# Kernel tuning notes

Measured on AMD Instinct MI355X. Metric: run time of the kernel, lower is better.

## Reference

```python
import jax, jax.numpy as jnp
import numpy as np

D_K = 24
ALPHA = 0.1
N_HEADS = 6
D_MODEL = 144
LN_EPS = 1e-5


def setup_inputs() -> dict:
    key = jax.random.key(0)
    ks = jax.random.split(key, 8)
    B, S = 8, 2048
    Q = jax.random.normal(ks[0], (B, S, D_MODEL), dtype=jnp.float32)
    K = jax.random.normal(ks[1], (B, N_HEADS, S, D_K), dtype=jnp.float32)
    V = jax.random.normal(ks[2], (B, N_HEADS, S, D_K), dtype=jnp.float32)
    attn_mask = jax.random.randint(ks[3], (B, S, S), 0, 2).astype(bool)
    Wq_w = jax.random.normal(ks[4], (D_MODEL, D_MODEL), dtype=jnp.float32) * 0.05
    Wq_b = jnp.zeros((D_MODEL,), dtype=jnp.float32)
    lin_w = jax.random.normal(ks[5], (D_MODEL, D_MODEL), dtype=jnp.float32) * 0.05
    lin_b = jnp.zeros((D_MODEL,), dtype=jnp.float32)
    ln_g = jnp.ones((D_MODEL,), dtype=jnp.float32)
    ln_b = jnp.zeros((D_MODEL,), dtype=jnp.float32)
    return {"Q": Q, "K": K, "V": V, "attn_mask": attn_mask,
            "Wq_w": Wq_w, "Wq_b": Wq_b, "lin_w": lin_w, "lin_b": lin_b,
            "ln_g": ln_g, "ln_b": ln_b}


def reference(Q, K, V, attn_mask, Wq_w, Wq_b, lin_w, lin_b, ln_g, ln_b):
    B, S, _ = Q.shape
    residual = Q
    # W_Q projection then head split: [B,S,D] -> [B,H,S,d_k]
    q = (Q @ Wq_w.T + Wq_b).reshape(B, S, N_HEADS, D_K).transpose(0, 2, 1, 3)
    # scores [B,H,S,Sk]; custom tanh activation instead of softmax
    scores = jnp.einsum('bhqd,bhkd->bhqk', q, K) / np.sqrt(D_K).astype(np.float32)
    attn = jnp.tanh(ALPHA * scores)
    # NOTE: original calls attn.masked_fill(...) non-inplace and drops the
    # result, so attn_mask has no effect. Faithfully ignored here.
    context = jnp.einsum('bhqk,bhkd->bhqd', attn, V)
    context = context.transpose(0, 2, 1, 3).reshape(B, S, N_HEADS * D_K)
    output = context @ lin_w.T + lin_b
    x = output + residual
    mu = jnp.mean(x, axis=-1, keepdims=True)
    var = jnp.var(x, axis=-1, keepdims=True)
    return (x - mu) / jnp.sqrt(var + LN_EPS) * ln_g + ln_b
```

## Files before the change

### kernel.cpp

```cpp
#include <hip/hip_runtime.h>
#include <hip/hip_bf16.h>

#define B_  8
#define S_  2048
#define H_  6
#define DK_ 24
#define DM_ 144

#define TK0  2.0412414523193153e-02f
#define TK1 -2.8350575726379381e-06f
#define TK2  4.7250959543965635e-10f
#define TK3 -7.9686705934386491e-14f

typedef __bf16 bf16x8 __attribute__((ext_vector_type(8)));
typedef __bf16 bf16x2 __attribute__((ext_vector_type(2)));
typedef float  f32x4  __attribute__((ext_vector_type(4)));

__device__ __forceinline__ unsigned short f2bf(float f) {
    return __builtin_bit_cast(unsigned short, (__bf16)f);
}
__device__ __forceinline__ uint pack2(float a, float b) {
    bf16x2 v; v[0] = (__bf16)a; v[1] = (__bf16)b;
    return __builtin_bit_cast(uint, v);
}
__device__ __forceinline__ float tanh_s(float c) {
    float t = c * c;
    float u = fmaf(t, TK3, TK2);
    u = fmaf(t, u, TK1);
    u = fmaf(t, u, TK0);
    return c * u;
}

__global__ __launch_bounds__(256)
void prep_w_kernel(const float* __restrict__ Wq, const float* __restrict__ Wqb,
                   const float* __restrict__ Wl, const float* __restrict__ lb,
                   ushort* __restrict__ Whq, ushort* __restrict__ Wlp) {
    int i = blockIdx.x * 256 + threadIdx.x;
    if (i < 30720) {
        int h = i / 5120, rem = i % 5120;
        int d = rem / 160, c = rem % 160;
        float v = 0.f;
        if (d < DK_) {
            if (c < DM_)       v = Wq[(h * DK_ + d) * DM_ + c];
            else if (c == DM_) v = Wqb[h * DK_ + d];
        }
        Whq[i] = f2bf(v);
    } else if (i < 53760) {
        int j = i - 30720;
        int r = j / 160, c = j % 160;
        float v = (c < DM_) ? Wl[r * DM_ + c] : (c == DM_ ? lb[r] : 0.f);
        Wlp[j] = f2bf(v);
    }
}

__global__ __launch_bounds__(256)
void prep_kv_kernel(const float* __restrict__ K, const float* __restrict__ V,
                    ushort* __restrict__ Ktt, ushort* __restrict__ Vtt) {
    __shared__ float sv[64 * 25];
    const int t = threadIdx.x;
    const int kt = blockIdx.x, h = blockIdx.y, b = blockIdx.z;
    const int bh = b * H_ + h;
    const size_t tile = (size_t)(bh * 32 + kt);
    const float4* Ks = (const float4*)(K + ((size_t)bh * S_ + kt * 64) * DK_);
    ushort* Ko = Ktt + tile * 2048;
    for (int idx = t; idx < 384; idx += 256) {
        int r = idx / 6, c4 = (idx % 6) * 4;
        float4 v = Ks[idx];
        ushort4 u; u.x = f2bf(v.x); u.y = f2bf(v.y); u.z = f2bf(v.z); u.w = f2bf(v.w);
        *(ushort4*)&Ko[r * 32 + c4] = u;
    }
    if (t < 64) { uint4 z = {0u,0u,0u,0u}; *(uint4*)&Ko[t * 32 + 24] = z; }
    const float4* Vs = (const float4*)(V + ((size_t)bh * S_ + kt * 64) * DK_);
    for (int idx = t; idx < 384; idx += 256) {
        int r = idx / 6, c4 = (idx % 6) * 4;
        *(float4*)&sv[r * 25 + c4] = Vs[idx];
    }
    __syncthreads();
    int d = t >> 3, s8 = (t & 7) * 8;
    uint4 o = {0u,0u,0u,0u};
    if (d < DK_) {
        o.x = pack2(sv[(s8 + 0) * 25 + d], sv[(s8 + 1) * 25 + d]);
        o.y = pack2(sv[(s8 + 2) * 25 + d], sv[(s8 + 3) * 25 + d]);
        o.z = pack2(sv[(s8 + 4) * 25 + d], sv[(s8 + 5) * 25 + d]);
        o.w = pack2(sv[(s8 + 6) * 25 + d], sv[(s8 + 7) * 25 + d]);
    }
    ((uint4*)Vtt)[tile * 256 + t] = o;
}

__global__ __launch_bounds__(256)
void attn_kernel(const float* __restrict__ Q, const ushort* __restrict__ Whq,
                 const ushort* __restrict__ Ktt, const ushort* __restrict__ Vtt,
                 float* __restrict__ out) {
    __shared__ __attribute__((aligned(16))) char smem[42496];
    ushort* s_q  = (ushort*)smem;
    ushort* s_k  = (ushort*)(smem + 10240);
    ushort* s_vt = (ushort*)(smem + 20480);
    ushort* s_p  = (ushort*)(smem + 29696);
    ushort* s_a  = (ushort*)(smem + 10240);
    ushort* s_w  = (ushort*)(smem + 31744);
    float*  s_ctx= (float*)(smem + 10240);

    const int t = threadIdx.x;
    const int w = t >> 6, n16 = t & 15, g = (t >> 4) & 3;
    const int qp = blockIdx.x, h = blockIdx.y, b = blockIdx.z;
    const int bh = b * H_ + h;
    const int row0 = qp * 128;

    const uint4* Kb = (const uint4*)(Ktt + (size_t)bh * 65536);
    const uint4* Vb = (const uint4*)(Vtt + (size_t)bh * 65536);
    uint4 kv = Kb[t], vv = Vb[t];

    const uint4* Ws = (const uint4*)(Whq + h * 5120);
    for (int idx = t; idx < 640; idx += 256) {
        int r = idx / 20, c8 = (idx % 20) * 8;
        *(uint4*)&s_w[r * 168 + c8] = Ws[idx];
    }
    const f32x4 zf = {0.f, 0.f, 0.f, 0.f};
#pragma unroll
    for (int pass = 0; pass < 2; ++pass) {
        const float4* Qs = (const float4*)(Q + ((size_t)b * S_ + row0 + pass * 64) * DM_);
        for (int idx = t; idx < 2304; idx += 256) {
            int r = idx / 36, c4 = (idx % 36) * 4;
            float4 v = Qs[idx];
            uint2 u; u.x = pack2(v.x, v.y); u.y = pack2(v.z, v.w);
            *(uint2*)&s_a[r * 168 + c4] = u;
        }
        if (t < 64) {
            uint4 pad = {0x00003F80u, 0u, 0u, 0u};
            uint4 z4  = {0u, 0u, 0u, 0u};
            *(uint4*)&s_a[t * 168 + 144] = pad;
            *(uint4*)&s_a[t * 168 + 152] = z4;
        }
        __syncthreads();
        f32x4 qa0 = zf, qa1 = zf;
#pragma unroll
        for (int ks = 0; ks < 5; ++ks) {
            bf16x8 av = *(const bf16x8*)&s_a[(w * 16 + n16) * 168 + ks * 32 + g * 8];
            bf16x8 b0 = *(const bf16x8*)&s_w[n16 * 168 + ks * 32 + g * 8];
            bf16x8 b1 = *(const bf16x8*)&s_w[(16 + n16) * 168 + ks * 32 + g * 8];
            qa0 = __builtin_amdgcn_mfma_f32_16x16x32_bf16(av, b0, qa0, 0, 0, 0);
            qa1 = __builtin_amdgcn_mfma_f32_16x16x32_bf16(av, b1, qa1, 0, 0, 0);
        }
#pragma unroll
        for (int reg = 0; reg < 4; ++reg) {
            int r = (pass * 64 + w * 16 + g * 4 + reg) * 40;
            s_q[r + n16]      = f2bf(qa0[reg]);
            s_q[r + 16 + n16] = f2bf(qa1[reg]);
        }
        __syncthreads();
    }

    const bf16x8 qf0 = *(const bf16x8*)&s_q[(w * 16 + n16) * 40 + g * 8];
    const bf16x8 qf1 = *(const bf16x8*)&s_q[(64 + w * 16 + n16) * 40 + g * 8];

    const int koff = (t >> 2) * 40 + (t & 3) * 8;
    const int voff = (t >> 3) * 72 + (t & 7) * 8;
    const int prow = (w * 16 + n16) * 72;

    f32x4 acc00 = zf, acc01 = zf, acc10 = zf, acc11 = zf;
    int p = 0;
    for (int kt = 0; kt < 32; ++kt) {
        *(uint4*)&s_k[p * 2560 + koff] = kv;
        *(uint4*)&s_vt[p * 2304 + voff] = vv;
        __syncthreads();
        {
            int nt = (kt + 1) & 31;
            kv = Kb[nt * 256 + t];
            vv = Vb[nt * 256 + t];
        }
        bf16x8 a0 = *(const bf16x8*)&s_k[p * 2560 + n16 * 40 + g * 8];
        bf16x8 a1 = *(const bf16x8*)&s_k[p * 2560 + (16 + n16) * 40 + g * 8];
        bf16x8 a2 = *(const bf16x8*)&s_k[p * 2560 + (32 + n16) * 40 + g * 8];
        bf16x8 a3 = *(const bf16x8*)&s_k[p * 2560 + (48 + n16) * 40 + g * 8];
        bf16x8 vb00 = *(const bf16x8*)&s_vt[p * 2304 + n16 * 72 + g * 8];
        bf16x8 vb01 = *(const bf16x8*)&s_vt[p * 2304 + (16 + n16) * 72 + g * 8];
        bf16x8 vb10 = *(const bf16x8*)&s_vt[p * 2304 + n16 * 72 + 32 + g * 8];
        bf16x8 vb11 = *(const bf16x8*)&s_vt[p * 2304 + (16 + n16) * 72 + 32 + g * 8];
        {
            f32x4 c0 = __builtin_amdgcn_mfma_f32_16x16x32_bf16(a0, qf0, zf, 0, 0, 0);
            f32x4 c1 = __builtin_amdgcn_mfma_f32_16x16x32_bf16(a1, qf0, zf, 0, 0, 0);
            f32x4 c2 = __builtin_amdgcn_mfma_f32_16x16x32_bf16(a2, qf0, zf, 0, 0, 0);
            f32x4 c3 = __builtin_amdgcn_mfma_f32_16x16x32_bf16(a3, qf0, zf, 0, 0, 0);
            uint2 u;
            u.x = pack2(tanh_s(c0[0]), tanh_s(c0[1]));
            u.y = pack2(tanh_s(c0[2]), tanh_s(c0[3]));
            *(uint2*)&s_p[prow + 0  + g * 4] = u;
            u.x = pack2(tanh_s(c1[0]), tanh_s(c1[1]));
            u.y = pack2(tanh_s(c1[2]), tanh_s(c1[3]));
            *(uint2*)&s_p[prow + 16 + g * 4] = u;
            u.x = pack2(tanh_s(c2[0]), tanh_s(c2[1]));
            u.y = pack2(tanh_s(c2[2]), tanh_s(c2[3]));
            *(uint2*)&s_p[prow + 32 + g * 4] = u;
            u.x = pack2(tanh_s(c3[0]), tanh_s(c3[1]));
            u.y = pack2(tanh_s(c3[2]), tanh_s(c3[3]));
            *(uint2*)&s_p[prow + 48 + g * 4] = u;
            bf16x8 ap0 = *(const bf16x8*)&s_p[prow + g * 8];
            acc00 = __builtin_amdgcn_mfma_f32_16x16x32_bf16(ap0, vb00, acc00, 0, 0, 0);
            acc01 = __builtin_amdgcn_mfma_f32_16x16x32_bf16(ap0, vb01, acc01, 0, 0, 0);
            bf16x8 ap1 = *(const bf16x8*)&s_p[prow + 32 + g * 8];
            acc00 = __builtin_amdgcn_mfma_f32_16x16x32_bf16(ap1, vb10, acc00, 0, 0, 0);
            acc01 = __builtin_amdgcn_mfma_f32_16x16x32_bf16(ap1, vb11, acc01, 0, 0, 0);
        }
        {
            f32x4 c0 = __builtin_amdgcn_mfma_f32_16x16x32_bf16(a0, qf1, zf, 0, 0, 0);
            f32x4 c1 = __builtin_amdgcn_mfma_f32_16x16x32_bf16(a1, qf1, zf, 0, 0, 0);
            f32x4 c2 = __builtin_amdgcn_mfma_f32_16x16x32_bf16(a2, qf1, zf, 0, 0, 0);
            f32x4 c3 = __builtin_amdgcn_mfma_f32_16x16x32_bf16(a3, qf1, zf, 0, 0, 0);
            uint2 u;
            u.x = pack2(tanh_s(c0[0]), tanh_s(c0[1]));
            u.y = pack2(tanh_s(c0[2]), tanh_s(c0[3]));
            *(uint2*)&s_p[prow + 0  + g * 4] = u;
            u.x = pack2(tanh_s(c1[0]), tanh_s(c1[1]));
            u.y = pack2(tanh_s(c1[2]), tanh_s(c1[3]));
            *(uint2*)&s_p[prow + 16 + g * 4] = u;
            u.x = pack2(tanh_s(c2[0]), tanh_s(c2[1]));
            u.y = pack2(tanh_s(c2[2]), tanh_s(c2[3]));
            *(uint2*)&s_p[prow + 32 + g * 4] = u;
            u.x = pack2(tanh_s(c3[0]), tanh_s(c3[1]));
            u.y = pack2(tanh_s(c3[2]), tanh_s(c3[3]));
            *(uint2*)&s_p[prow + 48 + g * 4] = u;
            bf16x8 ap0 = *(const bf16x8*)&s_p[prow + g * 8];
            acc10 = __builtin_amdgcn_mfma_f32_16x16x32_bf16(ap0, vb00, acc10, 0, 0, 0);
            acc11 = __builtin_amdgcn_mfma_f32_16x16x32_bf16(ap0, vb01, acc11, 0, 0, 0);
            bf16x8 ap1 = *(const bf16x8*)&s_p[prow + 32 + g * 8];
            acc10 = __builtin_amdgcn_mfma_f32_16x16x32_bf16(ap1, vb10, acc10, 0, 0, 0);
            acc11 = __builtin_amdgcn_mfma_f32_16x16x32_bf16(ap1, vb11, acc11, 0, 0, 0);
        }
        p ^= 1;
    }

    __syncthreads();
#pragma unroll
    for (int reg = 0; reg < 4; ++reg) {
        int row = w * 16 + g * 4 + reg;
        s_ctx[row * 28 + n16] = acc00[reg];
        if (n16 < 8) s_ctx[row * 28 + 16 + n16] = acc01[reg];
        s_ctx[(64 + row) * 28 + n16] = acc10[reg];
        if (n16 < 8) s_ctx[(64 + row) * 28 + 16 + n16] = acc11[reg];
    }
    __syncthreads();
    for (int idx = t; idx < 768; idx += 256) {
        int r = idx / 6, c = idx % 6;
        float4 v4 = *(const float4*)&s_ctx[r * 28 + c * 4];
        *(float4*)&out[((size_t)b * S_ + row0 + r) * DM_ + h * DK_ + c * 4] = v4;
    }
}

__global__ __launch_bounds__(512)
void outln_kernel(const float* __restrict__ Qres, const ushort* __restrict__ Wlp,
                  const float* __restrict__ lg, const float* __restrict__ lbeta,
                  float* __restrict__ io) {
    __shared__ __attribute__((aligned(16))) ushort s_a[64 * 168];
    __shared__ __attribute__((aligned(16))) ushort s_w[144 * 168];
    __shared__ float s_red[2][2][64];
    const int t = threadIdx.x;
    const int w = t >> 6, n16 = t & 15, g = (t >> 4) & 3;
    const int wq = w & 3, half = w >> 2;
    const int nt_base = half * 5, nt_cnt = half ? 4 : 5;
    const int row0 = blockIdx.x * 64;

    for (int idx = t; idx < 2304; idx += 512) {
        int r = idx / 36, c4 = (idx % 36) * 4;
        float4 v = *(const float4*)&io[(size_t)(row0 + r) * DM_ + c4];
        uint2 u; u.x = pack2(v.x, v.y); u.y = pack2(v.z, v.w);
        *(uint2*)&s_a[r * 168 + c4] = u;
    }
    if (t < 64) {
        uint4 pad = {0x00003F80u, 0u, 0u, 0u};
        uint4 z4  = {0u, 0u, 0u, 0u};
        *(uint4*)&s_a[t * 168 + 144] = pad;
        *(uint4*)&s_a[t * 168 + 152] = z4;
    }
    for (int idx = t; idx < 2880; idx += 512) {
        int r = idx / 20, c8 = (idx % 20) * 8;
        *(uint4*)&s_w[r * 168 + c8] = *(const uint4*)&Wlp[r * 160 + c8];
    }
    __syncthreads();

    f32x4 acc[5];
#pragma unroll
    for (int j = 0; j < 5; ++j) acc[j] = (f32x4){0.f, 0.f, 0.f, 0.f};
#pragma unroll
    for (int ks = 0; ks < 5; ++ks) {
        bf16x8 av = *(const bf16x8*)&s_a[(wq * 16 + n16) * 168 + ks * 32 + g * 8];
        for (int j = 0; j < nt_cnt; ++j) {
            bf16x8 bv = *(const bf16x8*)&s_w[((nt_base + j) * 16 + n16) * 168 + ks * 32 + g * 8];
            acc[j] = __builtin_amdgcn_mfma_f32_16x16x32_bf16(av, bv, acc[j], 0, 0, 0);
        }
    }
    float vals[5][4], s1[4] = {0, 0, 0, 0}, s2[4] = {0, 0, 0, 0};
    for (int j = 0; j < nt_cnt; ++j) {
        int d = (nt_base + j) * 16 + n16;
#pragma unroll
        for (int reg = 0; reg < 4; ++reg) {
            int row = row0 + wq * 16 + g * 4 + reg;
            float v = acc[j][reg] + Qres[(size_t)row * DM_ + d];
            vals[j][reg] = v;
            s1[reg] += v; s2[reg] = fmaf(v, v, s2[reg]);
        }
    }
#pragma unroll
    for (int off = 1; off < 16; off <<= 1) {
#pragma unroll
        for (int reg = 0; reg < 4; ++reg) {
            s1[reg] += __shfl_xor(s1[reg], off);
            s2[reg] += __shfl_xor(s2[reg], off);
        }
    }
    if (n16 == 0) {
#pragma unroll
        for (int reg = 0; reg < 4; ++reg) {
            int rr = wq * 16 + g * 4 + reg;
            s_red[half][0][rr] = s1[reg];
            s_red[half][1][rr] = s2[reg];
        }
    }
    __syncthreads();
    float mu[4], rs[4];
#pragma unroll
    for (int reg = 0; reg < 4; ++reg) {
        int rr = wq * 16 + g * 4 + reg;
        float S1 = s_red[0][0][rr] + s_red[1][0][rr];
        float S2 = s_red[0][1][rr] + s_red[1][1][rr];
        float m = S1 * (1.f / 144.f);
        mu[reg] = m;
        rs[reg] = rsqrtf(S2 * (1.f / 144.f) - m * m + 1e-5f);
    }
    for (int j = 0; j < nt_cnt; ++j) {
        int d = (nt_base + j) * 16 + n16;
        float gv = lg[d], bv = lbeta[d];
#pragma unroll
        for (int reg = 0; reg < 4; ++reg) {
            int row = row0 + wq * 16 + g * 4 + reg;
            io[(size_t)row * DM_ + d] = (vals[j][reg] - mu[reg]) * rs[reg] * gv + bv;
        }
    }
}

extern "C" void kernel_launch(void* const* d_in, const int* in_sizes, int n_in,
                              void* d_out, int out_size, void* d_ws, size_t ws_size,
                              hipStream_t stream) {
    const float* Q     = (const float*)d_in[0];
    const float* K     = (const float*)d_in[1];
    const float* V     = (const float*)d_in[2];
    const float* Wq_w  = (const float*)d_in[4];
    const float* Wq_b  = (const float*)d_in[5];
    const float* lin_w = (const float*)d_in[6];
    const float* lin_b = (const float*)d_in[7];
    const float* ln_g  = (const float*)d_in[8];
    const float* ln_b  = (const float*)d_in[9];
    float* out = (float*)d_out;

    ushort* Ktt = (ushort*)d_ws;
    ushort* Vtt = (ushort*)((char*)d_ws + 6291456);
    ushort* Whq = (ushort*)((char*)d_ws + 12582912);
    ushort* Wlp = (ushort*)((char*)d_ws + 12644352);

    prep_w_kernel<<<210, 256, 0, stream>>>(Wq_w, Wq_b, lin_w, lin_b, Whq, Wlp);
    prep_kv_kernel<<<dim3(32, H_, B_), 256, 0, stream>>>(K, V, Ktt, Vtt);
    attn_kernel<<<dim3(S_ / 128, H_, B_), 256, 0, stream>>>(Q, Whq, Ktt, Vtt, out);
    outln_kernel<<<(B_ * S_) / 64, 512, 0, stream>>>(Q, Wlp, ln_g, ln_b, out);
}
```

Before: 270.0 us.

## Load K/V fragments directly to registers and software-pipeline attention per wave

The attention loop stops staging K and V tiles through shared memory with block-wide barriers. Each wave now loads its MFMA fragments straight from global memory into double-buffered registers. A per-wave double-buffered P scratch lets the P·V MFMAs of one tile overlap the QK MFMAs of the next. The Q projection also reads Q and the weights directly from global memory, the tanh polynomial drops its highest-order term, and launch bounds request three blocks per CU. These changes remove barriers and LDS traffic, at the cost of more registers, redundant global loads per wave, and a slightly less accurate tanh.

Result: slower. 281.5 us (+4.3%).

```diff
diff --git a/kernel.cpp b/kernel.cpp
--- a/kernel.cpp
+++ b/kernel.cpp
@@ -10,12 +10,13 @@
 #define TK0  2.0412414523193153e-02f
 #define TK1 -2.8350575726379381e-06f
 #define TK2  4.7250959543965635e-10f
-#define TK3 -7.9686705934386491e-14f
 
 typedef __bf16 bf16x8 __attribute__((ext_vector_type(8)));
 typedef __bf16 bf16x2 __attribute__((ext_vector_type(2)));
 typedef float  f32x4  __attribute__((ext_vector_type(4)));
 
+#define MFMA_ __builtin_amdgcn_mfma_f32_16x16x32_bf16
+
 __device__ __forceinline__ unsigned short f2bf(float f) {
     return __builtin_bit_cast(unsigned short, (__bf16)f);
 }
@@ -25,8 +26,7 @@
 }
 __device__ __forceinline__ float tanh_s(float c) {
     float t = c * c;
-    float u = fmaf(t, TK3, TK2);
-    u = fmaf(t, u, TK1);
+    float u = fmaf(t, TK2, TK1);
     u = fmaf(t, u, TK0);
     return c * u;
 }
@@ -87,18 +87,77 @@
     ((uint4*)Vtt)[tile * 256 + t] = o;
 }
 
-__global__ __launch_bounds__(256)
+template<int PQ, bool DO_PV, bool PRE>
+__device__ __forceinline__ void attn_step(
+    int kt, const uint4* __restrict__ Kb4, const uint4* __restrict__ Vb4,
+    int koff, int voff, ushort* s_pw, int prow, int g,
+    const bf16x8& qf0, const bf16x8& qf1,
+    bf16x8 (&kf)[2][4], bf16x8 (&vf)[2][4],
+    f32x4& acc00, f32x4& acc01, f32x4& acc10, f32x4& acc11)
+{
+    constexpr int OP = 1 - PQ;
+    const f32x4 zf = {0.f, 0.f, 0.f, 0.f};
+    if (PRE) {
+        const int tb = ((kt + 1) & 31) * 256;
+#pragma unroll
+        for (int mt = 0; mt < 4; ++mt)
+            kf[OP][mt] = __builtin_bit_cast(bf16x8, Kb4[tb + mt * 64 + koff]);
+    }
+    bf16x8 ap00, ap01, ap10, ap11;
+    if (DO_PV) {
+        const ushort* pr = s_pw + OP * 2304 + prow;
+        ap00 = *(const bf16x8*)&pr[g * 8];
+        ap01 = *(const bf16x8*)&pr[32 + g * 8];
+        ap10 = *(const bf16x8*)&pr[1152 + g * 8];
+        ap11 = *(const bf16x8*)&pr[1152 + 32 + g * 8];
+    }
+    f32x4 c0[4], c1[4];
+#pragma unroll
+    for (int mt = 0; mt < 4; ++mt) c0[mt] = MFMA_(kf[PQ][mt], qf0, zf, 0, 0, 0);
+#pragma unroll
+    for (int mt = 0; mt < 4; ++mt) c1[mt] = MFMA_(kf[PQ][mt], qf1, zf, 0, 0, 0);
+    if (DO_PV) {
+        acc00 = MFMA_(ap00, vf[OP][0], acc00, 0, 0, 0);
+        acc00 = MFMA_(ap01, vf[OP][1], acc00, 0, 0, 0);
+        acc01 = MFMA_(ap00, vf[OP][2], acc01, 0, 0, 0);
+        acc01 = MFMA_(ap01, vf[OP][3], acc01, 0, 0, 0);
+        acc10 = MFMA_(ap10, vf[OP][0], acc10, 0, 0, 0);
+        acc10 = MFMA_(ap11, vf[OP][1], acc10, 0, 0, 0);
+        acc11 = MFMA_(ap10, vf[OP][2], acc11, 0, 0, 0);
+        acc11 = MFMA_(ap11, vf[OP][3], acc11, 0, 0, 0);
+    }
+    if (PRE) {
+        const int tb = ((kt + 1) & 31) * 256;
+#pragma unroll
+        for (int j = 0; j < 4; ++j)
+            vf[OP][j] = __builtin_bit_cast(bf16x8,
+                Vb4[tb + (j >> 1) * 128 + (j & 1) * 4 + voff]);
+    }
+    ushort* pw = s_pw + PQ * 2304 + prow;
+#pragma unroll
+    for (int mt = 0; mt < 4; ++mt) {
+        uint2 u;
+        u.x = pack2(tanh_s(c0[mt][0]), tanh_s(c0[mt][1]));
+        u.y = pack2(tanh_s(c0[mt][2]), tanh_s(c0[mt][3]));
+        *(uint2*)&pw[mt * 16 + g * 4] = u;
+    }
+#pragma unroll
+    for (int mt = 0; mt < 4; ++mt) {
+        uint2 u;
+        u.x = pack2(tanh_s(c1[mt][0]), tanh_s(c1[mt][1]));
+        u.y = pack2(tanh_s(c1[mt][2]), tanh_s(c1[mt][3]));
+        *(uint2*)&pw[1152 + mt * 16 + g * 4] = u;
+    }
+}
+
+__global__ __launch_bounds__(256, 3)
 void attn_kernel(const float* __restrict__ Q, const ushort* __restrict__ Whq,
                  const ushort* __restrict__ Ktt, const ushort* __restrict__ Vtt,
                  float* __restrict__ out) {
-    __shared__ __attribute__((aligned(16))) char smem[42496];
-    ushort* s_q  = (ushort*)smem;
-    ushort* s_k  = (ushort*)(smem + 10240);
-    ushort* s_vt = (ushort*)(smem + 20480);
-    ushort* s_p  = (ushort*)(smem + 29696);
-    ushort* s_a  = (ushort*)(smem + 10240);
-    ushort* s_w  = (ushort*)(smem + 31744);
-    float*  s_ctx= (float*)(smem + 10240);
+    __shared__ __attribute__((aligned(16))) char smem[47104];
+    ushort* s_q = (ushort*)smem;
+    ushort* s_p = (ushort*)(smem + 10240);
+    float*  s_ctx = (float*)(smem + 10240);
 
     const int t = threadIdx.x;
     const int w = t >> 6, n16 = t & 15, g = (t >> 4) & 3;
@@ -106,40 +165,44 @@
     const int bh = b * H_ + h;
     const int row0 = qp * 128;
 
-    const uint4* Kb = (const uint4*)(Ktt + (size_t)bh * 65536);
-    const uint4* Vb = (const uint4*)(Vtt + (size_t)bh * 65536);
-    uint4 kv = Kb[t], vv = Vb[t];
-
-    const uint4* Ws = (const uint4*)(Whq + h * 5120);
-    for (int idx = t; idx < 640; idx += 256) {
-        int r = idx / 20, c8 = (idx % 20) * 8;
-        *(uint4*)&s_w[r * 168 + c8] = Ws[idx];
-    }
+    const uint4* Kb4 = (const uint4*)Ktt + (size_t)bh * 8192;
+    const uint4* Vb4 = (const uint4*)Vtt + (size_t)bh * 8192;
+    const int koff = n16 * 4 + g;
+    const int voff = n16 * 8 + g;
+
+    bf16x8 kf[2][4], vf[2][4];
+#pragma unroll
+    for (int mt = 0; mt < 4; ++mt)
+        kf[0][mt] = __builtin_bit_cast(bf16x8, Kb4[mt * 64 + koff]);
+#pragma unroll
+    for (int j = 0; j < 4; ++j)
+        vf[0][j] = __builtin_bit_cast(bf16x8, Vb4[(j >> 1) * 128 + (j & 1) * 4 + voff]);
+
     const f32x4 zf = {0.f, 0.f, 0.f, 0.f};
+    const uint4* Wh4 = (const uint4*)Whq + h * 640;
 #pragma unroll
     for (int pass = 0; pass < 2; ++pass) {
-        const float4* Qs = (const float4*)(Q + ((size_t)b * S_ + row0 + pass * 64) * DM_);
-        for (int idx = t; idx < 2304; idx += 256) {
-            int r = idx / 36, c4 = (idx % 36) * 4;
-            float4 v = Qs[idx];
-            uint2 u; u.x = pack2(v.x, v.y); u.y = pack2(v.z, v.w);
-            *(uint2*)&s_a[r * 168 + c4] = u;
-        }
-        if (t < 64) {
-            uint4 pad = {0x00003F80u, 0u, 0u, 0u};
-            uint4 z4  = {0u, 0u, 0u, 0u};
-            *(uint4*)&s_a[t * 168 + 144] = pad;
-            *(uint4*)&s_a[t * 168 + 152] = z4;
-        }
-        __syncthreads();
+        const float* Qr = Q + (size_t)(b * S_ + row0 + pass * 64 + w * 16 + n16) * DM_;
         f32x4 qa0 = zf, qa1 = zf;
 #pragma unroll
         for (int ks = 0; ks < 5; ++ks) {
-            bf16x8 av = *(const bf16x8*)&s_a[(w * 16 + n16) * 168 + ks * 32 + g * 8];
-            bf16x8 b0 = *(const bf16x8*)&s_w[n16 * 168 + ks * 32 + g * 8];
-            bf16x8 b1 = *(const bf16x8*)&s_w[(16 + n16) * 168 + ks * 32 + g * 8];
-            qa0 = __builtin_amdgcn_mfma_f32_16x16x32_bf16(av, b0, qa0, 0, 0, 0);
-            qa1 = __builtin_amdgcn_mfma_f32_16x16x32_bf16(av, b1, qa1, 0, 0, 0);
+            bf16x8 av;
+            if (ks < 4 || g < 2) {
+                float4 f0 = *(const float4*)&Qr[ks * 32 + g * 8];
+                float4 f1 = *(const float4*)&Qr[ks * 32 + g * 8 + 4];
+                uint4 u;
+                u.x = pack2(f0.x, f0.y); u.y = pack2(f0.z, f0.w);
+                u.z = pack2(f1.x, f1.y); u.w = pack2(f1.z, f1.w);
+                av = __builtin_bit_cast(bf16x8, u);
+            } else {
+                uint4 u = {0u, 0u, 0u, 0u};
+                if (g == 2) u.x = 0x00003F80u;
+                av = __builtin_bit_cast(bf16x8, u);
+            }
+            bf16x8 bv0 = __builtin_bit_cast(bf16x8, Wh4[n16 * 20 + ks * 4 + g]);
+            bf16x8 bv1 = __builtin_bit_cast(bf16x8, Wh4[(16 + n16) * 20 + ks * 4 + g]);
+            qa0 = MFMA_(av, bv0, qa0, 0, 0, 0);
+            qa1 = MFMA_(av, bv1, qa1, 0, 0, 0);
         }
 #pragma unroll
         for (int reg = 0; reg < 4; ++reg) {
@@ -147,86 +210,38 @@
             s_q[r + n16]      = f2bf(qa0[reg]);
             s_q[r + 16 + n16] = f2bf(qa1[reg]);
         }
-        __syncthreads();
-    }
-
+    }
     const bf16x8 qf0 = *(const bf16x8*)&s_q[(w * 16 + n16) * 40 + g * 8];
     const bf16x8 qf1 = *(const bf16x8*)&s_q[(64 + w * 16 + n16) * 40 + g * 8];
 
-    const int koff = (t >> 2) * 40 + (t & 3) * 8;
-    const int voff = (t >> 3) * 72 + (t & 7) * 8;
-    const int prow = (w * 16 + n16) * 72;
-
+    ushort* s_pw = s_p + w * 4608;
+    const int prow = n16 * 72;
     f32x4 acc00 = zf, acc01 = zf, acc10 = zf, acc11 = zf;
-    int p = 0;
-    for (int kt = 0; kt < 32; ++kt) {
-        *(uint4*)&s_k[p * 2560 + koff] = kv;
-        *(uint4*)&s_vt[p * 2304 + voff] = vv;
-        __syncthreads();
-        {
-            int nt = (kt + 1) & 31;
-            kv = Kb[nt * 256 + t];
-            vv = Vb[nt * 256 + t];
-        }
-        bf16x8 a0 = *(const bf16x8*)&s_k[p * 2560 + n16 * 40 + g * 8];
-        bf16x8 a1 = *(const bf16x8*)&s_k[p * 2560 + (16 + n16) * 40 + g * 8];
-        bf16x8 a2 = *(const bf16x8*)&s_k[p * 2560 + (32 + n16) * 40 + g * 8];
-        bf16x8 a3 = *(const bf16x8*)&s_k[p * 2560 + (48 + n16) * 40 + g * 8];
-        bf16x8 vb00 = *(const bf16x8*)&s_vt[p * 2304 + n16 * 72 + g * 8];
-        bf16x8 vb01 = *(const bf16x8*)&s_vt[p * 2304 + (16 + n16) * 72 + g * 8];
-        bf16x8 vb10 = *(const bf16x8*)&s_vt[p * 2304 + n16 * 72 + 32 + g * 8];
-        bf16x8 vb11 = *(const bf16x8*)&s_vt[p * 2304 + (16 + n16) * 72 + 32 + g * 8];
-        {
-            f32x4 c0 = __builtin_amdgcn_mfma_f32_16x16x32_bf16(a0, qf0, zf, 0, 0, 0);
-            f32x4 c1 = __builtin_amdgcn_mfma_f32_16x16x32_bf16(a1, qf0, zf, 0, 0, 0);
-            f32x4 c2 = __builtin_amdgcn_mfma_f32_16x16x32_bf16(a2, qf0, zf, 0, 0, 0);
-            f32x4 c3 = __builtin_amdgcn_mfma_f32_16x16x32_bf16(a3, qf0, zf, 0, 0, 0);
-            uint2 u;
-            u.x = pack2(tanh_s(c0[0]), tanh_s(c0[1]));
-            u.y = pack2(tanh_s(c0[2]), tanh_s(c0[3]));
-            *(uint2*)&s_p[prow + 0  + g * 4] = u;
-            u.x = pack2(tanh_s(c1[0]), tanh_s(c1[1]));
-            u.y = pack2(tanh_s(c1[2]), tanh_s(c1[3]));
-            *(uint2*)&s_p[prow + 16 + g * 4] = u;
-            u.x = pack2(tanh_s(c2[0]), tanh_s(c2[1]));
-            u.y = pack2(tanh_s(c2[2]), tanh_s(c2[3]));
-            *(uint2*)&s_p[prow + 32 + g * 4] = u;
-            u.x = pack2(tanh_s(c3[0]), tanh_s(c3[1]));
-            u.y = pack2(tanh_s(c3[2]), tanh_s(c3[3]));
-            *(uint2*)&s_p[prow + 48 + g * 4] = u;
-            bf16x8 ap0 = *(const bf16x8*)&s_p[prow + g * 8];
-            acc00 = __builtin_amdgcn_mfma_f32_16x16x32_bf16(ap0, vb00, acc00, 0, 0, 0);
-            acc01 = __builtin_amdgcn_mfma_f32_16x16x32_bf16(ap0, vb01, acc01, 0, 0, 0);
-            bf16x8 ap1 = *(const bf16x8*)&s_p[prow + 32 + g * 8];
-            acc00 = __builtin_amdgcn_mfma_f32_16x16x32_bf16(ap1, vb10, acc00, 0, 0, 0);
-            acc01 = __builtin_amdgcn_mfma_f32_16x16x32_bf16(ap1, vb11, acc01, 0, 0, 0);
-        }
-        {
-            f32x4 c0 = __builtin_amdgcn_mfma_f32_16x16x32_bf16(a0, qf1, zf, 0, 0, 0);
-            f32x4 c1 = __builtin_amdgcn_mfma_f32_16x16x32_bf16(a1, qf1, zf, 0, 0, 0);
-            f32x4 c2 = __builtin_amdgcn_mfma_f32_16x16x32_bf16(a2, qf1, zf, 0, 0, 0);
-            f32x4 c3 = __builtin_amdgcn_mfma_f32_16x16x32_bf16(a3, qf1, zf, 0, 0, 0);
-            uint2 u;
-            u.x = pack2(tanh_s(c0[0]), tanh_s(c0[1]));
-            u.y = pack2(tanh_s(c0[2]), tanh_s(c0[3]));
-            *(uint2*)&s_p[prow + 0  + g * 4] = u;
-            u.x = pack2(tanh_s(c1[0]), tanh_s(c1[1]));
-            u.y = pack2(tanh_s(c1[2]), tanh_s(c1[3]));
-            *(uint2*)&s_p[prow + 16 + g * 4] = u;
-            u.x = pack2(tanh_s(c2[0]), tanh_s(c2[1]));
-            u.y = pack2(tanh_s(c2[2]), tanh_s(c2[3]));
-            *(uint2*)&s_p[prow + 32 + g * 4] = u;
-            u.x = pack2(tanh_s(c3[0]), tanh_s(c3[1]));
-            u.y = pack2(tanh_s(c3[2]), tanh_s(c3[3]));
-            *(uint2*)&s_p[prow + 48 + g * 4] = u;
-            bf16x8 ap0 = *(const bf16x8*)&s_p[prow + g * 8];
-            acc10 = __builtin_amdgcn_mfma_f32_16x16x32_bf16(ap0, vb00, acc10, 0, 0, 0);
-            acc11 = __builtin_amdgcn_mfma_f32_16x16x32_bf16(ap0, vb01, acc11, 0, 0, 0);
-            bf16x8 ap1 = *(const bf16x8*)&s_p[prow + 32 + g * 8];
-            acc10 = __builtin_amdgcn_mfma_f32_16x16x32_bf16(ap1, vb10, acc10, 0, 0, 0);
-            acc11 = __builtin_amdgcn_mfma_f32_16x16x32_bf16(ap1, vb11, acc11, 0, 0, 0);
-        }
-        p ^= 1;
+
+    attn_step<0, false, true>(0, Kb4, Vb4, koff, voff, s_pw, prow, g,
+                              qf0, qf1, kf, vf, acc00, acc01, acc10, acc11);
+    for (int kt = 1; kt < 31; kt += 2) {
+        attn_step<1, true, true>(kt, Kb4, Vb4, koff, voff, s_pw, prow, g,
+                                 qf0, qf1, kf, vf, acc00, acc01, acc10, acc11);
+        attn_step<0, true, true>(kt + 1, Kb4, Vb4, koff, voff, s_pw, prow, g,
+                                 qf0, qf1, kf, vf, acc00, acc01, acc10, acc11);
+    }
+    attn_step<1, true, false>(31, Kb4, Vb4, koff, voff, s_pw, prow, g,
+                              qf0, qf1, kf, vf, acc00, acc01, acc10, acc11);
+    {
+        const ushort* pr = s_pw + 2304 + prow;
+        bf16x8 ap00 = *(const bf16x8*)&pr[g * 8];
+        bf16x8 ap01 = *(const bf16x8*)&pr[32 + g * 8];
+        bf16x8 ap10 = *(const bf16x8*)&pr[1152 + g * 8];
+        bf16x8 ap11 = *(const bf16x8*)&pr[1152 + 32 + g * 8];
+        acc00 = MFMA_(ap00, vf[1][0], acc00, 0, 0, 0);
+        acc00 = MFMA_(ap01, vf[1][1], acc00, 0, 0, 0);
+        acc01 = MFMA_(ap00, vf[1][2], acc01, 0, 0, 0);
+        acc01 = MFMA_(ap01, vf[1][3], acc01, 0, 0, 0);
+        acc10 = MFMA_(ap10, vf[1][0], acc10, 0, 0, 0);
+        acc10 = MFMA_(ap11, vf[1][1], acc10, 0, 0, 0);
+        acc11 = MFMA_(ap10, vf[1][2], acc11, 0, 0, 0);
+        acc11 = MFMA_(ap11, vf[1][3], acc11, 0, 0, 0);
     }
 
     __syncthreads();
@@ -285,7 +300,7 @@
         bf16x8 av = *(const bf16x8*)&s_a[(wq * 16 + n16) * 168 + ks * 32 + g * 8];
         for (int j = 0; j < nt_cnt; ++j) {
             bf16x8 bv = *(const bf16x8*)&s_w[((nt_base + j) * 16 + n16) * 168 + ks * 32 + g * 8];
-            acc[j] = __builtin_amdgcn_mfma_f32_16x16x32_bf16(av, bv, acc[j], 0, 0, 0);
+            acc[j] = MFMA_(av, bv, acc[j], 0, 0, 0);
         }
     }
     float vals[5][4], s1[4] = {0, 0, 0, 0}, s2[4] = {0, 0, 0, 0};
```

## Use 8 waves per attention block, one 16-row query tile per wave

Applied to the files above, without the earlier changes.

The attention kernel moves from 256 to 512 threads. Each of the 8 waves now owns one 16-row query tile instead of two, and each wave has a private P scratch buffer. K and V tile staging is split so half the threads load K and half load V. The Q projection now reads Q and Wq directly from global memory into MFMA fragments, which removes the shared staging and two barriers. The tanh polynomial also drops its cubic term, cutting per-element ALU work at some cost in accuracy. The goal is more parallelism and fewer serialized steps per wave, traded against higher register and LDS pressure per block.

New measurement: 268.4 us. About the same (-0.6%).

```diff
diff --git a/kernel.cpp b/kernel.cpp
--- a/kernel.cpp
+++ b/kernel.cpp
@@ -10,12 +10,13 @@
 #define TK0  2.0412414523193153e-02f
 #define TK1 -2.8350575726379381e-06f
 #define TK2  4.7250959543965635e-10f
-#define TK3 -7.9686705934386491e-14f
 
 typedef __bf16 bf16x8 __attribute__((ext_vector_type(8)));
 typedef __bf16 bf16x2 __attribute__((ext_vector_type(2)));
 typedef float  f32x4  __attribute__((ext_vector_type(4)));
 
+#define MFMA_ __builtin_amdgcn_mfma_f32_16x16x32_bf16
+
 __device__ __forceinline__ unsigned short f2bf(float f) {
     return __builtin_bit_cast(unsigned short, (__bf16)f);
 }
@@ -25,8 +26,7 @@
 }
 __device__ __forceinline__ float tanh_s(float c) {
     float t = c * c;
-    float u = fmaf(t, TK3, TK2);
-    u = fmaf(t, u, TK1);
+    float u = fmaf(t, TK2, TK1);
     u = fmaf(t, u, TK0);
     return c * u;
 }
@@ -87,18 +87,16 @@
     ((uint4*)Vtt)[tile * 256 + t] = o;
 }
 
-__global__ __launch_bounds__(256)
+__global__ __launch_bounds__(512, 6)
 void attn_kernel(const float* __restrict__ Q, const ushort* __restrict__ Whq,
                  const ushort* __restrict__ Ktt, const ushort* __restrict__ Vtt,
                  float* __restrict__ out) {
-    __shared__ __attribute__((aligned(16))) char smem[42496];
+    __shared__ __attribute__((aligned(16))) char smem[48128];
     ushort* s_q  = (ushort*)smem;
     ushort* s_k  = (ushort*)(smem + 10240);
     ushort* s_vt = (ushort*)(smem + 20480);
     ushort* s_p  = (ushort*)(smem + 29696);
-    ushort* s_a  = (ushort*)(smem + 10240);
-    ushort* s_w  = (ushort*)(smem + 31744);
-    float*  s_ctx= (float*)(smem + 10240);
+    float*  s_ctx = (float*)smem;
 
     const int t = threadIdx.x;
     const int w = t >> 6, n16 = t & 15, g = (t >> 4) & 3;
@@ -106,126 +104,91 @@
     const int bh = b * H_ + h;
     const int row0 = qp * 128;
 
-    const uint4* Kb = (const uint4*)(Ktt + (size_t)bh * 65536);
-    const uint4* Vb = (const uint4*)(Vtt + (size_t)bh * 65536);
-    uint4 kv = Kb[t], vv = Vb[t];
-
-    const uint4* Ws = (const uint4*)(Whq + h * 5120);
-    for (int idx = t; idx < 640; idx += 256) {
-        int r = idx / 20, c8 = (idx % 20) * 8;
-        *(uint4*)&s_w[r * 168 + c8] = Ws[idx];
-    }
+    const uint4* Kb4 = (const uint4*)Ktt + (size_t)bh * 8192;
+    const uint4* Vb4 = (const uint4*)Vtt + (size_t)bh * 8192;
+
+    const int t2 = t & 255;
+    const int stoff = (t < 256) ? ((t2 >> 2) * 40 + (t2 & 3) * 8)
+                                : ((t2 >> 3) * 72 + (t2 & 7) * 8);
+    uint4 sreg = (t < 256) ? Kb4[t2] : Vb4[t2];
+
     const f32x4 zf = {0.f, 0.f, 0.f, 0.f};
-#pragma unroll
-    for (int pass = 0; pass < 2; ++pass) {
-        const float4* Qs = (const float4*)(Q + ((size_t)b * S_ + row0 + pass * 64) * DM_);
-        for (int idx = t; idx < 2304; idx += 256) {
-            int r = idx / 36, c4 = (idx % 36) * 4;
-            float4 v = Qs[idx];
-            uint2 u; u.x = pack2(v.x, v.y); u.y = pack2(v.z, v.w);
-            *(uint2*)&s_a[r * 168 + c4] = u;
-        }
-        if (t < 64) {
-            uint4 pad = {0x00003F80u, 0u, 0u, 0u};
-            uint4 z4  = {0u, 0u, 0u, 0u};
-            *(uint4*)&s_a[t * 168 + 144] = pad;
-            *(uint4*)&s_a[t * 168 + 152] = z4;
-        }
-        __syncthreads();
+    const uint4* Wh4 = (const uint4*)Whq + h * 640;
+    {
+        const float* Qr = Q + (size_t)(b * S_ + row0 + w * 16 + n16) * DM_;
         f32x4 qa0 = zf, qa1 = zf;
 #pragma unroll
         for (int ks = 0; ks < 5; ++ks) {
-            bf16x8 av = *(const bf16x8*)&s_a[(w * 16 + n16) * 168 + ks * 32 + g * 8];
-            bf16x8 b0 = *(const bf16x8*)&s_w[n16 * 168 + ks * 32 + g * 8];
-            bf16x8 b1 = *(const bf16x8*)&s_w[(16 + n16) * 168 + ks * 32 + g * 8];
-            qa0 = __builtin_amdgcn_mfma_f32_16x16x32_bf16(av, b0, qa0, 0, 0, 0);
-            qa1 = __builtin_amdgcn_mfma_f32_16x16x32_bf16(av, b1, qa1, 0, 0, 0);
-        }
-#pragma unroll
-        for (int reg = 0; reg < 4; ++reg) {
-            int r = (pass * 64 + w * 16 + g * 4 + reg) * 40;
+            bf16x8 av;
+            if (ks < 4 || g < 2) {
+                float4 f0 = *(const float4*)&Qr[ks * 32 + g * 8];
+                float4 f1 = *(const float4*)&Qr[ks * 32 + g * 8 + 4];
+                uint4 u;
+                u.x = pack2(f0.x, f0.y); u.y = pack2(f0.z, f0.w);
+                u.z = pack2(f1.x, f1.y); u.w = pack2(f1.z, f1.w);
+                av = __builtin_bit_cast(bf16x8, u);
+            } else {
+                uint4 u = {0u, 0u, 0u, 0u};
+                if (g == 2) u.x = 0x00003F80u;
+                av = __builtin_bit_cast(bf16x8, u);
+            }
+            bf16x8 bv0 = __builtin_bit_cast(bf16x8, Wh4[n16 * 20 + ks * 4 + g]);
+            bf16x8 bv1 = __builtin_bit_cast(bf16x8, Wh4[(16 + n16) * 20 + ks * 4 + g]);
+            qa0 = MFMA_(av, bv0, qa0, 0, 0, 0);
+            qa1 = MFMA_(av, bv1, qa1, 0, 0, 0);
+        }
+#pragma unroll
+        for (int reg = 0; reg < 4; ++reg) {
+            int r = (w * 16 + g * 4 + reg) * 40;
             s_q[r + n16]      = f2bf(qa0[reg]);
             s_q[r + 16 + n16] = f2bf(qa1[reg]);
         }
-        __syncthreads();
-    }
-
-    const bf16x8 qf0 = *(const bf16x8*)&s_q[(w * 16 + n16) * 40 + g * 8];
-    const bf16x8 qf1 = *(const bf16x8*)&s_q[(64 + w * 16 + n16) * 40 + g * 8];
-
-    const int koff = (t >> 2) * 40 + (t & 3) * 8;
-    const int voff = (t >> 3) * 72 + (t & 7) * 8;
-    const int prow = (w * 16 + n16) * 72;
-
-    f32x4 acc00 = zf, acc01 = zf, acc10 = zf, acc11 = zf;
+    }
+    const bf16x8 qf = *(const bf16x8*)&s_q[(w * 16 + n16) * 40 + g * 8];
+
+    ushort* s_pw = s_p + w * 1152;
+    const int prow = n16 * 72;
+    f32x4 acc0 = zf, acc1 = zf;
     int p = 0;
     for (int kt = 0; kt < 32; ++kt) {
-        *(uint4*)&s_k[p * 2560 + koff] = kv;
-        *(uint4*)&s_vt[p * 2304 + voff] = vv;
+        if (t < 256) *(uint4*)&s_k[p * 2560 + stoff] = sreg;
+        else         *(uint4*)&s_vt[p * 2304 + stoff] = sreg;
         __syncthreads();
         {
-            int nt = (kt + 1) & 31;
-            kv = Kb[nt * 256 + t];
-            vv = Vb[nt * 256 + t];
+            int nt = ((kt + 1) & 31) * 256;
+            sreg = (t < 256) ? Kb4[nt + t2] : Vb4[nt + t2];
         }
         bf16x8 a0 = *(const bf16x8*)&s_k[p * 2560 + n16 * 40 + g * 8];
         bf16x8 a1 = *(const bf16x8*)&s_k[p * 2560 + (16 + n16) * 40 + g * 8];
         bf16x8 a2 = *(const bf16x8*)&s_k[p * 2560 + (32 + n16) * 40 + g * 8];
         bf16x8 a3 = *(const bf16x8*)&s_k[p * 2560 + (48 + n16) * 40 + g * 8];
+        f32x4 c0 = MFMA_(a0, qf, zf, 0, 0, 0);
+        f32x4 c1 = MFMA_(a1, qf, zf, 0, 0, 0);
+        f32x4 c2 = MFMA_(a2, qf, zf, 0, 0, 0);
+        f32x4 c3 = MFMA_(a3, qf, zf, 0, 0, 0);
+        uint2 u;
+        u.x = pack2(tanh_s(c0[0]), tanh_s(c0[1]));
+        u.y = pack2(tanh_s(c0[2]), tanh_s(c0[3]));
+        *(uint2*)&s_pw[prow + 0  + g * 4] = u;
+        u.x = pack2(tanh_s(c1[0]), tanh_s(c1[1]));
+        u.y = pack2(tanh_s(c1[2]), tanh_s(c1[3]));
+        *(uint2*)&s_pw[prow + 16 + g * 4] = u;
+        u.x = pack2(tanh_s(c2[0]), tanh_s(c2[1]));
+        u.y = pack2(tanh_s(c2[2]), tanh_s(c2[3]));
+        *(uint2*)&s_pw[prow + 32 + g * 4] = u;
+        u.x = pack2(tanh_s(c3[0]), tanh_s(c3[1]));
+        u.y = pack2(tanh_s(c3[2]), tanh_s(c3[3]));
+        *(uint2*)&s_pw[prow + 48 + g * 4] = u;
+        bf16x8 ap0 = *(const bf16x8*)&s_pw[prow + g * 8];
+        bf16x8 ap1 = *(const bf16x8*)&s_pw[prow + 32 + g * 8];
         bf16x8 vb00 = *(const bf16x8*)&s_vt[p * 2304 + n16 * 72 + g * 8];
-        bf16x8 vb01 = *(const bf16x8*)&s_vt[p * 2304 + (16 + n16) * 72 + g * 8];
-        bf16x8 vb10 = *(const bf16x8*)&s_vt[p * 2304 + n16 * 72 + 32 + g * 8];
+        bf16x8 vb01 = *(const bf16x8*)&s_vt[p * 2304 + n16 * 72 + 32 + g * 8];
+        bf16x8 vb10 = *(const bf16x8*)&s_vt[p * 2304 + (16 + n16) * 72 + g * 8];
         bf16x8 vb11 = *(const bf16x8*)&s_vt[p * 2304 + (16 + n16) * 72 + 32 + g * 8];
-        {
-            f32x4 c0 = __builtin_amdgcn_mfma_f32_16x16x32_bf16(a0, qf0, zf, 0, 0, 0);
-            f32x4 c1 = __builtin_amdgcn_mfma_f32_16x16x32_bf16(a1, qf0, zf, 0, 0, 0);
-            f32x4 c2 = __builtin_amdgcn_mfma_f32_16x16x32_bf16(a2, qf0, zf, 0, 0, 0);
-            f32x4 c3 = __builtin_amdgcn_mfma_f32_16x16x32_bf16(a3, qf0, zf, 0, 0, 0);
-            uint2 u;
-            u.x = pack2(tanh_s(c0[0]), tanh_s(c0[1]));
-            u.y = pack2(tanh_s(c0[2]), tanh_s(c0[3]));
-            *(uint2*)&s_p[prow + 0  + g * 4] = u;
-            u.x = pack2(tanh_s(c1[0]), tanh_s(c1[1]));
-            u.y = pack2(tanh_s(c1[2]), tanh_s(c1[3]));
-            *(uint2*)&s_p[prow + 16 + g * 4] = u;
-            u.x = pack2(tanh_s(c2[0]), tanh_s(c2[1]));
-            u.y = pack2(tanh_s(c2[2]), tanh_s(c2[3]));
-            *(uint2*)&s_p[prow + 32 + g * 4] = u;
-            u.x = pack2(tanh_s(c3[0]), tanh_s(c3[1]));
-            u.y = pack2(tanh_s(c3[2]), tanh_s(c3[3]));
-            *(uint2*)&s_p[prow + 48 + g * 4] = u;
-            bf16x8 ap0 = *(const bf16x8*)&s_p[prow + g * 8];
-            acc00 = __builtin_amdgcn_mfma_f32_16x16x32_bf16(ap0, vb00, acc00, 0, 0, 0);
-            acc01 = __builtin_amdgcn_mfma_f32_16x16x32_bf16(ap0, vb01, acc01, 0, 0, 0);
-            bf16x8 ap1 = *(const bf16x8*)&s_p[prow + 32 + g * 8];
-            acc00 = __builtin_amdgcn_mfma_f32_16x16x32_bf16(ap1, vb10, acc00, 0, 0, 0);
-            acc01 = __builtin_amdgcn_mfma_f32_16x16x32_bf16(ap1, vb11, acc01, 0, 0, 0);
-        }
-        {
-            f32x4 c0 = __builtin_amdgcn_mfma_f32_16x16x32_bf16(a0, qf1, zf, 0, 0, 0);
-            f32x4 c1 = __builtin_amdgcn_mfma_f32_16x16x32_bf16(a1, qf1, zf, 0, 0, 0);
-            f32x4 c2 = __builtin_amdgcn_mfma_f32_16x16x32_bf16(a2, qf1, zf, 0, 0, 0);
-            f32x4 c3 = __builtin_amdgcn_mfma_f32_16x16x32_bf16(a3, qf1, zf, 0, 0, 0);
-            uint2 u;
-            u.x = pack2(tanh_s(c0[0]), tanh_s(c0[1]));
-            u.y = pack2(tanh_s(c0[2]), tanh_s(c0[3]));
-            *(uint2*)&s_p[prow + 0  + g * 4] = u;
-            u.x = pack2(tanh_s(c1[0]), tanh_s(c1[1]));
-            u.y = pack2(tanh_s(c1[2]), tanh_s(c1[3]));
-            *(uint2*)&s_p[prow + 16 + g * 4] = u;
-            u.x = pack2(tanh_s(c2[0]), tanh_s(c2[1]));
-            u.y = pack2(tanh_s(c2[2]), tanh_s(c2[3]));
-            *(uint2*)&s_p[prow + 32 + g * 4] = u;
-            u.x = pack2(tanh_s(c3[0]), tanh_s(c3[1]));
-            u.y = pack2(tanh_s(c3[2]), tanh_s(c3[3]));
-            *(uint2*)&s_p[prow + 48 + g * 4] = u;
-            bf16x8 ap0 = *(const bf16x8*)&s_p[prow + g * 8];
-            acc10 = __builtin_amdgcn_mfma_f32_16x16x32_bf16(ap0, vb00, acc10, 0, 0, 0);
-            acc11 = __builtin_amdgcn_mfma_f32_16x16x32_bf16(ap0, vb01, acc11, 0, 0, 0);
-            bf16x8 ap1 = *(const bf16x8*)&s_p[prow + 32 + g * 8];
-            acc10 = __builtin_amdgcn_mfma_f32_16x16x32_bf16(ap1, vb10, acc10, 0, 0, 0);
-            acc11 = __builtin_amdgcn_mfma_f32_16x16x32_bf16(ap1, vb11, acc11, 0, 0, 0);
-        }
+        acc0 = MFMA_(ap0, vb00, acc0, 0, 0, 0);
+        acc0 = MFMA_(ap1, vb01, acc0, 0, 0, 0);
+        acc1 = MFMA_(ap0, vb10, acc1, 0, 0, 0);
+        acc1 = MFMA_(ap1, vb11, acc1, 0, 0, 0);
         p ^= 1;
     }
 
@@ -233,13 +196,11 @@
 #pragma unroll
     for (int reg = 0; reg < 4; ++reg) {
         int row = w * 16 + g * 4 + reg;
-        s_ctx[row * 28 + n16] = acc00[reg];
-        if (n16 < 8) s_ctx[row * 28 + 16 + n16] = acc01[reg];
-        s_ctx[(64 + row) * 28 + n16] = acc10[reg];
-        if (n16 < 8) s_ctx[(64 + row) * 28 + 16 + n16] = acc11[reg];
-    }
-    __syncthreads();
-    for (int idx = t; idx < 768; idx += 256) {
+        s_ctx[row * 28 + n16] = acc0[reg];
+        if (n16 < 8) s_ctx[row * 28 + 16 + n16] = acc1[reg];
+    }
+    __syncthreads();
+    for (int idx = t; idx < 768; idx += 512) {
         int r = idx / 6, c = idx % 6;
         float4 v4 = *(const float4*)&s_ctx[r * 28 + c * 4];
         *(float4*)&out[((size_t)b * S_ + row0 + r) * DM_ + h * DK_ + c * 4] = v4;
@@ -285,7 +246,7 @@
         bf16x8 av = *(const bf16x8*)&s_a[(wq * 16 + n16) * 168 + ks * 32 + g * 8];
         for (int j = 0; j < nt_cnt; ++j) {
             bf16x8 bv = *(const bf16x8*)&s_w[((nt_base + j) * 16 + n16) * 168 + ks * 32 + g * 8];
-            acc[j] = __builtin_amdgcn_mfma_f32_16x16x32_bf16(av, bv, acc[j], 0, 0, 0);
+            acc[j] = MFMA_(av, bv, acc[j], 0, 0, 0);
         }
     }
     float vals[5][4], s1[4] = {0, 0, 0, 0}, s2[4] = {0, 0, 0, 0};
@@ -358,6 +319,6 @@
 
     prep_w_kernel<<<210, 256, 0, stream>>>(Wq_w, Wq_b, lin_w, lin_b, Whq, Wlp);
     prep_kv_kernel<<<dim3(32, H_, B_), 256, 0, stream>>>(K, V, Ktt, Vtt);
-    attn_kernel<<<dim3(S_ / 128, H_, B_), 256, 0, stream>>>(Q, Whq, Ktt, Vtt, out);
+    attn_kernel<<<dim3(S_ / 128, H_, B_), 512, 0, stream>>>(Q, Whq, Ktt, Vtt, out);
     outln_kernel<<<(B_ * S_) / 64, 512, 0, stream>>>(Q, Wlp, ln_g, ln_b, out);
 }
```
